# Kernel optimization log

Hardware: AMD Instinct MI355X
Metric: run time of the kernel (lower is better)

## Reference

```python
import jax, jax.numpy as jnp
import numpy as np


def _proj(x_flat, W, scale, bias):
    # x_flat: [B, C, N]; 1x1 conv == per-pixel channel matmul, then eval-mode BN (affine) + ReLU
    y = jnp.einsum('oc,bcn->bon', W, x_flat)
    return jax.nn.relu(y * scale[None, :, None] + bias[None, :, None])


def setup_inputs() -> dict:
    key = jax.random.key(0)
    ks = jax.random.split(key, 11)
    B, C, H, W = 4, 256, 64, 64
    inp = {
        'query_feats': jax.random.normal(ks[0], (B, C, H, W), jnp.float32),
        'key_feats': jax.random.normal(ks[1], (B, C, H, W), jnp.float32),
        'Wq': jax.random.normal(ks[2], (C, C), jnp.float32) * (1.0 / np.sqrt(C)),
        'Wk': jax.random.normal(ks[3], (C, C), jnp.float32) * (1.0 / np.sqrt(C)),
        'Wv': jax.random.normal(ks[4], (C, C), jnp.float32) * (1.0 / np.sqrt(C)),
        'scale_q': jax.random.uniform(ks[5], (C,), jnp.float32, 0.5, 1.5),
        'bias_q': jax.random.normal(ks[6], (C,), jnp.float32) * 0.1,
        'scale_k': jax.random.uniform(ks[7], (C,), jnp.float32, 0.5, 1.5),
        'bias_k': jax.random.normal(ks[8], (C,), jnp.float32) * 0.1,
        'scale_v': jax.random.uniform(ks[9], (C,), jnp.float32, 0.5, 1.5),
        'bias_v': jax.random.normal(ks[10], (C,), jnp.float32) * 0.1,
    }
    return inp


def reference(query_feats, key_feats, Wq, Wk, Wv, scale_q, bias_q, scale_k, bias_k, scale_v, bias_v):
    B, C, H, W = query_feats.shape
    qf = query_feats.reshape(B, C, H * W)
    kf = key_feats.reshape(B, C, H * W)

    q = _proj(qf, Wq, scale_q, bias_q)           # [B, C, Nq]
    k = _proj(kf, Wk, scale_k, bias_k)           # [B, C, Nk]
    v = _proj(kf, Wv, scale_v, bias_v)           # [B, C, Nk]

    sim = jnp.einsum('bcq,bck->bqk', q, k) * (C ** -0.5)  # [B, Nq, Nk]
    attn = jax.nn.softmax(sim, axis=-1)
    ctx = jnp.einsum('bqk,bck->bcq', attn, v)              # [B, C, Nq]
    return ctx.reshape(B, C, H, W)
```

## Files before the change

### kernel.cpp

```cpp
#include <hip/hip_runtime.h>
#include <math.h>

#define CDIM 256
#define NPIX 4096
#define BATCH 4
#define QB 64
#define KB 32

typedef __attribute__((ext_vector_type(8))) short short8;
typedef __attribute__((ext_vector_type(4))) float f32x4;
#define MFMA(a, b, c) __builtin_amdgcn_mfma_f32_16x16x32_bf16((a), (b), (c), 0, 0, 0)

__device__ __forceinline__ unsigned short f2bf(float f) {
    union { float f; unsigned int u; } v; v.f = f;
    unsigned int u = v.u;
    return (unsigned short)((u + 0x7FFFu + ((u >> 16) & 1u)) >> 16);
}
__device__ __forceinline__ float bf2f(unsigned short h) {
    union { unsigned int u; float f; } v; v.u = ((unsigned int)h) << 16;
    return v.f;
}

__global__ __launch_bounds__(256) void proj_kernel(
    const float* __restrict__ qf, const float* __restrict__ kf,
    const float* __restrict__ Wq, const float* __restrict__ Wk, const float* __restrict__ Wv,
    const float* __restrict__ sq, const float* __restrict__ bq,
    const float* __restrict__ sk, const float* __restrict__ bk,
    const float* __restrict__ sv, const float* __restrict__ bv,
    unsigned short* __restrict__ Qth, unsigned short* __restrict__ Qtl,
    unsigned short* __restrict__ Kth, unsigned short* __restrict__ Ktl,
    unsigned short* __restrict__ Vh,  unsigned short* __restrict__ Vl)
{
    const int n0 = blockIdx.x * 64;
    const int o0 = blockIdx.y * 64;
    const int z  = blockIdx.z;
    const int which = z % 3;
    const int b     = z / 3;

    const float* W; const float* x; const float* sc; const float* bi;
    unsigned short* dh; unsigned short* dl;
    if (which == 0)      { W = Wq; x = qf; sc = sq; bi = bq; dh = Qth; dl = Qtl; }
    else if (which == 1) { W = Wk; x = kf; sc = sk; bi = bk; dh = Kth; dl = Ktl; }
    else                 { W = Wv; x = kf; sc = sv; bi = bv; dh = Vh;  dl = Vl;  }

    __shared__ float Wt[32][68];
    __shared__ float Xt[32][68];

    const int t  = threadIdx.x;
    const int to = t >> 4;
    const int tn = t & 15;

    const int w_oi  = t >> 2;
    const int w_cc0 = (t & 3) * 8;
    const int x_ci  = t >> 3;
    const int x_no  = (t & 7) * 8;

    float acc[4][4];
#pragma unroll
    for (int i = 0; i < 4; ++i)
#pragma unroll
        for (int j = 0; j < 4; ++j) acc[i][j] = 0.f;

    for (int c0 = 0; c0 < CDIM; c0 += 32) {
        float4 wv[2], xv[2];
#pragma unroll
        for (int v = 0; v < 2; ++v)
            wv[v] = *reinterpret_cast<const float4*>(
                &W[(size_t)(o0 + w_oi) * CDIM + c0 + w_cc0 + 4 * v]);
#pragma unroll
        for (int v = 0; v < 2; ++v)
            xv[v] = *reinterpret_cast<const float4*>(
                &x[((size_t)(b * CDIM + c0 + x_ci)) * NPIX + n0 + x_no + 4 * v]);
        __syncthreads();
#pragma unroll
        for (int v = 0; v < 2; ++v) {
            Wt[w_cc0 + 4 * v + 0][w_oi] = wv[v].x;
            Wt[w_cc0 + 4 * v + 1][w_oi] = wv[v].y;
            Wt[w_cc0 + 4 * v + 2][w_oi] = wv[v].z;
            Wt[w_cc0 + 4 * v + 3][w_oi] = wv[v].w;
            *reinterpret_cast<float4*>(&Xt[x_ci][x_no + 4 * v]) = xv[v];
        }
        __syncthreads();
#pragma unroll
        for (int cc = 0; cc < 32; ++cc) {
            float4 a = *reinterpret_cast<const float4*>(&Wt[cc][4 * to]);
            float4 c = *reinterpret_cast<const float4*>(&Xt[cc][4 * tn]);
            float wa[4] = {a.x, a.y, a.z, a.w};
            float xa[4] = {c.x, c.y, c.z, c.w};
#pragma unroll
            for (int i = 0; i < 4; ++i)
#pragma unroll
                for (int j = 0; j < 4; ++j)
                    acc[i][j] = fmaf(wa[i], xa[j], acc[i][j]);
        }
        __syncthreads();
    }

    unsigned short hi[4][4], lo[4][4];
#pragma unroll
    for (int i = 0; i < 4; ++i) {
        const int o = o0 + 4 * to + i;
        const float s = sc[o], bb = bi[o];
#pragma unroll
        for (int j = 0; j < 4; ++j) {
            float val = fmaxf(fmaf(acc[i][j], s, bb), 0.f);
            unsigned short h = f2bf(val);
            hi[i][j] = h;
            lo[i][j] = f2bf(val - bf2f(h));
        }
    }

    if (which < 2) {
#pragma unroll
        for (int j = 0; j < 4; ++j) {
            const size_t addr = ((size_t)b * NPIX + n0 + 4 * tn + j) * CDIM + o0 + 4 * to;
            ushort4 h4 = make_ushort4(hi[0][j], hi[1][j], hi[2][j], hi[3][j]);
            ushort4 l4 = make_ushort4(lo[0][j], lo[1][j], lo[2][j], lo[3][j]);
            *reinterpret_cast<ushort4*>(&dh[addr]) = h4;
            *reinterpret_cast<ushort4*>(&dl[addr]) = l4;
        }
    } else {
#pragma unroll
        for (int i = 0; i < 4; ++i) {
            const size_t addr = ((size_t)b * CDIM + o0 + 4 * to + i) * NPIX + n0 + 4 * tn;
            ushort4 h4 = make_ushort4(hi[i][0], hi[i][1], hi[i][2], hi[i][3]);
            ushort4 l4 = make_ushort4(lo[i][0], lo[i][1], lo[i][2], lo[i][3]);
            *reinterpret_cast<ushort4*>(&dh[addr]) = h4;
            *reinterpret_cast<ushort4*>(&dl[addr]) = l4;
        }
    }
}

__global__ __launch_bounds__(512, 2) void flash_kernel(
    const unsigned short* __restrict__ Qth, const unsigned short* __restrict__ Qtl,
    const unsigned short* __restrict__ Kth, const unsigned short* __restrict__ Ktl,
    const unsigned short* __restrict__ Vh,  const unsigned short* __restrict__ Vl,
    float* __restrict__ out)
{
    const int bid  = blockIdx.x;
    const int virt = ((bid & 7) << 5) | (bid >> 3);
    const int b    = virt >> 6;
    const int qb   = (virt & 63) * QB;

    __shared__ unsigned short Ksh[KB][264], Ksl[KB][264];
    __shared__ unsigned short Vsh[CDIM][40], Vsl[CDIM][40];
    __shared__ unsigned short Phs[QB][40],  Pls[QB][40];
    __shared__ float Msh[2][QB], Ssh2[2][QB], Rsh[QB], Linv[QB];

    const int t    = threadIdx.x;
    const int w    = t >> 6;
    const int lane = t & 63;
    const int g    = lane >> 4;
    const int li   = lane & 15;

    const int smq = w & 3, snk = w >> 2;
    const int pqf = w & 3, pch = w >> 2;

    const int krow = t >> 4, kcol = (t & 15) * 16;
    const int vrow = t >> 1, vcol = (t & 1) * 16;

    short8 qh[8], ql[8];
    {
        const size_t qbase = ((size_t)b * NPIX + qb + smq * 16 + li) * CDIM + g * 8;
#pragma unroll
        for (int cs = 0; cs < 8; ++cs) {
            qh[cs] = *reinterpret_cast<const short8*>(&Qth[qbase + cs * 32]);
            ql[cs] = *reinterpret_cast<const short8*>(&Qtl[qbase + cs * 32]);
        }
    }

    f32x4 O[8];
#pragma unroll
    for (int fi = 0; fi < 8; ++fi) O[fi] = (f32x4){0.f, 0.f, 0.f, 0.f};

    float m_run[4], l_run[4];
#pragma unroll
    for (int r = 0; r < 4; ++r) { m_run[r] = -INFINITY; l_run[r] = 0.f; }

    const float scl = 0.0625f;

    uint4 rKh0, rKh1, rKl0, rKl1, rVh0, rVh1, rVl0, rVl1;
    const size_t kgbase = ((size_t)b * NPIX + krow) * CDIM + kcol;
    const size_t vgbase = ((size_t)b * CDIM + vrow) * NPIX + vcol;

    {
        const size_t ka = kgbase;
        rKh0 = *reinterpret_cast<const uint4*>(&Kth[ka]);
        rKh1 = *reinterpret_cast<const uint4*>(&Kth[ka + 8]);
        rKl0 = *reinterpret_cast<const uint4*>(&Ktl[ka]);
        rKl1 = *reinterpret_cast<const uint4*>(&Ktl[ka + 8]);
        const size_t va = vgbase;
        rVh0 = *reinterpret_cast<const uint4*>(&Vh[va]);
        rVh1 = *reinterpret_cast<const uint4*>(&Vh[va + 8]);
        rVl0 = *reinterpret_cast<const uint4*>(&Vl[va]);
        rVl1 = *reinterpret_cast<const uint4*>(&Vl[va + 8]);
    }

    const int NT = NPIX / KB;
    for (int it = 0; it < NT; ++it) {
        *reinterpret_cast<uint4*>(&Ksh[krow][kcol])     = rKh0;
        *reinterpret_cast<uint4*>(&Ksh[krow][kcol + 8]) = rKh1;
        *reinterpret_cast<uint4*>(&Ksl[krow][kcol])     = rKl0;
        *reinterpret_cast<uint4*>(&Ksl[krow][kcol + 8]) = rKl1;
        *reinterpret_cast<uint4*>(&Vsh[vrow][vcol])     = rVh0;
        *reinterpret_cast<uint4*>(&Vsh[vrow][vcol + 8]) = rVh1;
        *reinterpret_cast<uint4*>(&Vsl[vrow][vcol])     = rVl0;
        *reinterpret_cast<uint4*>(&Vsl[vrow][vcol + 8]) = rVl1;
        __syncthreads();

        f32x4 sacc = (f32x4){0.f, 0.f, 0.f, 0.f};
#pragma unroll
        for (int cs = 0; cs < 8; ++cs) {
            short8 kbh = *reinterpret_cast<const short8*>(&Ksh[snk * 16 + li][cs * 32 + g * 8]);
            short8 kbl = *reinterpret_cast<const short8*>(&Ksl[snk * 16 + li][cs * 32 + g * 8]);
            sacc = MFMA(qh[cs], kbh, sacc);
            sacc = MFMA(ql[cs], kbh, sacc);
            sacc = MFMA(qh[cs], kbl, sacc);
        }

        {
            const int ktn = (it + 1 < NT) ? (it + 1) * KB : 0;
            const size_t ka = kgbase + (size_t)ktn * CDIM;
            rKh0 = *reinterpret_cast<const uint4*>(&Kth[ka]);
            rKh1 = *reinterpret_cast<const uint4*>(&Kth[ka + 8]);
            rKl0 = *reinterpret_cast<const uint4*>(&Ktl[ka]);
            rKl1 = *reinterpret_cast<const uint4*>(&Ktl[ka + 8]);
            const size_t va = vgbase + ktn;
            rVh0 = *reinterpret_cast<const uint4*>(&Vh[va]);
            rVh1 = *reinterpret_cast<const uint4*>(&Vh[va + 8]);
            rVl0 = *reinterpret_cast<const uint4*>(&Vl[va]);
            rVl1 = *reinterpret_cast<const uint4*>(&Vl[va + 8]);
        }

        float sv[4], mx[4];
#pragma unroll
        for (int r = 0; r < 4; ++r) { sv[r] = sacc[r] * scl; mx[r] = sv[r]; }
#pragma unroll
        for (int d = 1; d < 16; d <<= 1)
#pragma unroll
            for (int r = 0; r < 4; ++r) mx[r] = fmaxf(mx[r], __shfl_xor(mx[r], d, 64));

        if (li == 0) {
#pragma unroll
            for (int r = 0; r < 4; ++r) Msh[snk][smq * 16 + g * 4 + r] = mx[r];
        }
        __syncthreads();

        float p[4], resc[4], psum[4];
#pragma unroll
        for (int r = 0; r < 4; ++r) {
            const int q = smq * 16 + g * 4 + r;
            const float mt = fmaxf(Msh[0][q], Msh[1][q]);
            const float mn = fmaxf(m_run[r], mt);
            resc[r] = __expf(m_run[r] - mn);
            m_run[r] = mn;
            p[r] = __expf(sv[r] - mn);
            psum[r] = p[r];
        }
#pragma unroll
        for (int d = 1; d < 16; d <<= 1)
#pragma unroll
            for (int r = 0; r < 4; ++r) psum[r] += __shfl_xor(psum[r], d, 64);

#pragma unroll
        for (int r = 0; r < 4; ++r) {
            const int q = smq * 16 + g * 4 + r;
            unsigned short ph = f2bf(p[r]);
            Phs[q][snk * 16 + li] = ph;
            Pls[q][snk * 16 + li] = f2bf(p[r] - bf2f(ph));
        }
        if (li == 0) {
#pragma unroll
            for (int r = 0; r < 4; ++r) {
                const int q = smq * 16 + g * 4 + r;
                Ssh2[snk][q] = psum[r];
                if (snk == 0) Rsh[q] = resc[r];
            }
        }
        __syncthreads();

#pragma unroll
        for (int r = 0; r < 4; ++r) {
            const int q = smq * 16 + g * 4 + r;
            l_run[r] = l_run[r] * resc[r] + Ssh2[0][q] + Ssh2[1][q];
        }

        const float rf = Rsh[pqf * 16 + li];
        short8 pa = *reinterpret_cast<const short8*>(&Phs[pqf * 16 + li][g * 8]);
        short8 pb = *reinterpret_cast<const short8*>(&Pls[pqf * 16 + li][g * 8]);
#pragma unroll
        for (int fi = 0; fi < 8; ++fi) {
            O[fi] = O[fi] * rf;
            const int crow = (pch * 8 + fi) * 16 + li;
            short8 va = *reinterpret_cast<const short8*>(&Vsh[crow][g * 8]);
            short8 vb = *reinterpret_cast<const short8*>(&Vsl[crow][g * 8]);
            O[fi] = MFMA(va, pa, O[fi]);
            O[fi] = MFMA(vb, pa, O[fi]);
            O[fi] = MFMA(va, pb, O[fi]);
        }
        __syncthreads();
    }

    if (snk == 0 && li == 0) {
#pragma unroll
        for (int r = 0; r < 4; ++r)
            Linv[smq * 16 + g * 4 + r] = 1.0f / l_run[r];
    }
    __syncthreads();

    const float linv = Linv[pqf * 16 + li];
#pragma unroll
    for (int fi = 0; fi < 8; ++fi) {
#pragma unroll
        for (int r = 0; r < 4; ++r) {
            const int c = (pch * 8 + fi) * 16 + g * 4 + r;
            out[((size_t)(b * CDIM + c)) * NPIX + qb + pqf * 16 + li] = O[fi][r] * linv;
        }
    }
}

extern "C" void kernel_launch(void* const* d_in, const int* in_sizes, int n_in,
                              void* d_out, int out_size, void* d_ws, size_t ws_size,
                              hipStream_t stream)
{
    const float* qf = (const float*)d_in[0];
    const float* kf = (const float*)d_in[1];
    const float* Wq = (const float*)d_in[2];
    const float* Wk = (const float*)d_in[3];
    const float* Wv = (const float*)d_in[4];
    const float* sq = (const float*)d_in[5];
    const float* bq = (const float*)d_in[6];
    const float* sk = (const float*)d_in[7];
    const float* bk = (const float*)d_in[8];
    const float* sv = (const float*)d_in[9];
    const float* bv = (const float*)d_in[10];
    float* out = (float*)d_out;

    const size_t plane = (size_t)BATCH * CDIM * NPIX;
    unsigned short* ws = (unsigned short*)d_ws;
    unsigned short* Qth = ws;
    unsigned short* Qtl = ws + plane;
    unsigned short* Kth = ws + 2 * plane;
    unsigned short* Ktl = ws + 3 * plane;
    unsigned short* Vh  = ws + 4 * plane;
    unsigned short* Vl  = ws + 5 * plane;

    dim3 gp(NPIX / 64, CDIM / 64, 3 * BATCH);
    proj_kernel<<<gp, 256, 0, stream>>>(qf, kf, Wq, Wk, Wv, sq, bq, sk, bk, sv, bv,
                                        Qth, Qtl, Kth, Ktl, Vh, Vl);

    flash_kernel<<<dim3(256), 512, 0, stream>>>(Qth, Qtl, Kth, Ktl, Vh, Vl, out);
}
```

Before: 590.3 us.

## Split KV range across two blocks with merge kernel and swizzle V shared layout

Splits the key/value sequence into two halves so the flash kernel launches 512 blocks instead of 256, writing unnormalized partial outputs plus running max and sum to workspace. A separate merge kernel then combines the two partials with log-sum-exp rescaling. The launch bound is raised to 4 blocks per SM, and the V shared tile drops its padding in favour of an XOR swizzle to avoid bank conflicts. This fills more compute units on a 256-CU GPU, at the cost of extra global traffic for the partials and an additional kernel launch. It falls back to the old path if the workspace is too small.

```diff
diff --git a/kernel.cpp b/kernel.cpp
--- a/kernel.cpp
+++ b/kernel.cpp
@@ -6,6 +6,7 @@
 #define BATCH 4
 #define QB 64
 #define KB 32
+#define KVHALF 2048
 
 typedef __attribute__((ext_vector_type(8))) short short8;
 typedef __attribute__((ext_vector_type(4))) float f32x4;
@@ -131,19 +132,30 @@
     }
 }
 
-__global__ __launch_bounds__(512, 2) void flash_kernel(
+__global__ __launch_bounds__(512, 4) void flash_kernel(
     const unsigned short* __restrict__ Qth, const unsigned short* __restrict__ Qtl,
     const unsigned short* __restrict__ Kth, const unsigned short* __restrict__ Ktl,
     const unsigned short* __restrict__ Vh,  const unsigned short* __restrict__ Vl,
-    float* __restrict__ out)
+    float* __restrict__ Op, float* __restrict__ Mp, float* __restrict__ Lp,
+    float* __restrict__ out, int split)
 {
-    const int bid  = blockIdx.x;
-    const int virt = ((bid & 7) << 5) | (bid >> 3);
-    const int b    = virt >> 6;
-    const int qb   = (virt & 63) * QB;
+    const int bid = blockIdx.x;
+    int qt, b, kv, ntiles;
+    if (split) {
+        const int virt = ((bid & 7) << 6) | (bid >> 3);
+        qt = virt & 63;
+        const int bkv = virt >> 6;
+        b = bkv >> 1; kv = bkv & 1; ntiles = KVHALF / KB;
+    } else {
+        const int virt = ((bid & 7) << 5) | (bid >> 3);
+        qt = virt & 63; b = virt >> 6; kv = 0; ntiles = NPIX / KB;
+    }
+    const int qb = qt * QB;
+    const int k0 = kv * KVHALF;
+    const int pb = b * 64 + qt;
 
     __shared__ unsigned short Ksh[KB][264], Ksl[KB][264];
-    __shared__ unsigned short Vsh[CDIM][40], Vsl[CDIM][40];
+    __shared__ unsigned short Vsh[CDIM][32], Vsl[CDIM][32];
     __shared__ unsigned short Phs[QB][40],  Pls[QB][40];
     __shared__ float Msh[2][QB], Ssh2[2][QB], Rsh[QB], Linv[QB];
 
@@ -158,6 +170,10 @@
 
     const int krow = t >> 4, kcol = (t & 15) * 16;
     const int vrow = t >> 1, vcol = (t & 1) * 16;
+    const int vsw  = (vrow >> 2) & 3;
+    const int vp0  = ((2 * (t & 1) + 0) ^ vsw) * 8;
+    const int vp1  = ((2 * (t & 1) + 1) ^ vsw) * 8;
+    const int pg   = (g ^ ((li >> 2) & 3)) * 8;
 
     short8 qh[8], ql[8];
     {
@@ -180,32 +196,29 @@
     const float scl = 0.0625f;
 
     uint4 rKh0, rKh1, rKl0, rKl1, rVh0, rVh1, rVl0, rVl1;
-    const size_t kgbase = ((size_t)b * NPIX + krow) * CDIM + kcol;
-    const size_t vgbase = ((size_t)b * CDIM + vrow) * NPIX + vcol;
-
-    {
-        const size_t ka = kgbase;
-        rKh0 = *reinterpret_cast<const uint4*>(&Kth[ka]);
-        rKh1 = *reinterpret_cast<const uint4*>(&Kth[ka + 8]);
-        rKl0 = *reinterpret_cast<const uint4*>(&Ktl[ka]);
-        rKl1 = *reinterpret_cast<const uint4*>(&Ktl[ka + 8]);
-        const size_t va = vgbase;
-        rVh0 = *reinterpret_cast<const uint4*>(&Vh[va]);
-        rVh1 = *reinterpret_cast<const uint4*>(&Vh[va + 8]);
-        rVl0 = *reinterpret_cast<const uint4*>(&Vl[va]);
-        rVl1 = *reinterpret_cast<const uint4*>(&Vl[va + 8]);
-    }
-
-    const int NT = NPIX / KB;
-    for (int it = 0; it < NT; ++it) {
+    const size_t kgbase = ((size_t)b * NPIX + k0 + krow) * CDIM + kcol;
+    const size_t vgbase = ((size_t)(b * CDIM + vrow)) * NPIX + k0 + vcol;
+
+    {
+        rKh0 = *reinterpret_cast<const uint4*>(&Kth[kgbase]);
+        rKh1 = *reinterpret_cast<const uint4*>(&Kth[kgbase + 8]);
+        rKl0 = *reinterpret_cast<const uint4*>(&Ktl[kgbase]);
+        rKl1 = *reinterpret_cast<const uint4*>(&Ktl[kgbase + 8]);
+        rVh0 = *reinterpret_cast<const uint4*>(&Vh[vgbase]);
+        rVh1 = *reinterpret_cast<const uint4*>(&Vh[vgbase + 8]);
+        rVl0 = *reinterpret_cast<const uint4*>(&Vl[vgbase]);
+        rVl1 = *reinterpret_cast<const uint4*>(&Vl[vgbase + 8]);
+    }
+
+    for (int it = 0; it < ntiles; ++it) {
         *reinterpret_cast<uint4*>(&Ksh[krow][kcol])     = rKh0;
         *reinterpret_cast<uint4*>(&Ksh[krow][kcol + 8]) = rKh1;
         *reinterpret_cast<uint4*>(&Ksl[krow][kcol])     = rKl0;
         *reinterpret_cast<uint4*>(&Ksl[krow][kcol + 8]) = rKl1;
-        *reinterpret_cast<uint4*>(&Vsh[vrow][vcol])     = rVh0;
-        *reinterpret_cast<uint4*>(&Vsh[vrow][vcol + 8]) = rVh1;
-        *reinterpret_cast<uint4*>(&Vsl[vrow][vcol])     = rVl0;
-        *reinterpret_cast<uint4*>(&Vsl[vrow][vcol + 8]) = rVl1;
+        *reinterpret_cast<uint4*>(&Vsh[vrow][vp0])      = rVh0;
+        *reinterpret_cast<uint4*>(&Vsh[vrow][vp1])      = rVh1;
+        *reinterpret_cast<uint4*>(&Vsl[vrow][vp0])      = rVl0;
+        *reinterpret_cast<uint4*>(&Vsl[vrow][vp1])      = rVl1;
         __syncthreads();
 
         f32x4 sacc = (f32x4){0.f, 0.f, 0.f, 0.f};
@@ -219,7 +232,7 @@
         }
 
         {
-            const int ktn = (it + 1 < NT) ? (it + 1) * KB : 0;
+            const int ktn = (it + 1 < ntiles) ? (it + 1) * KB : 0;
             const size_t ka = kgbase + (size_t)ktn * CDIM;
             rKh0 = *reinterpret_cast<const uint4*>(&Kth[ka]);
             rKh1 = *reinterpret_cast<const uint4*>(&Kth[ka + 8]);
@@ -287,36 +300,100 @@
 
         const float rf = Rsh[pqf * 16 + li];
         short8 pa = *reinterpret_cast<const short8*>(&Phs[pqf * 16 + li][g * 8]);
-        short8 pb = *reinterpret_cast<const short8*>(&Pls[pqf * 16 + li][g * 8]);
+        short8 pb2 = *reinterpret_cast<const short8*>(&Pls[pqf * 16 + li][g * 8]);
 #pragma unroll
         for (int fi = 0; fi < 8; ++fi) {
             O[fi] = O[fi] * rf;
             const int crow = (pch * 8 + fi) * 16 + li;
-            short8 va = *reinterpret_cast<const short8*>(&Vsh[crow][g * 8]);
-            short8 vb = *reinterpret_cast<const short8*>(&Vsl[crow][g * 8]);
+            short8 va = *reinterpret_cast<const short8*>(&Vsh[crow][pg]);
+            short8 vb = *reinterpret_cast<const short8*>(&Vsl[crow][pg]);
             O[fi] = MFMA(va, pa, O[fi]);
             O[fi] = MFMA(vb, pa, O[fi]);
-            O[fi] = MFMA(va, pb, O[fi]);
-        }
-        __syncthreads();
-    }
-
-    if (snk == 0 && li == 0) {
-#pragma unroll
-        for (int r = 0; r < 4; ++r)
-            Linv[smq * 16 + g * 4 + r] = 1.0f / l_run[r];
-    }
-    __syncthreads();
-
-    const float linv = Linv[pqf * 16 + li];
-#pragma unroll
-    for (int fi = 0; fi < 8; ++fi) {
-#pragma unroll
-        for (int r = 0; r < 4; ++r) {
-            const int c = (pch * 8 + fi) * 16 + g * 4 + r;
-            out[((size_t)(b * CDIM + c)) * NPIX + qb + pqf * 16 + li] = O[fi][r] * linv;
-        }
-    }
+            O[fi] = MFMA(va, pb2, O[fi]);
+        }
+        __syncthreads();
+    }
+
+    if (split) {
+        const size_t obase = ((size_t)(kv * 256 + pb)) * 256;
+#pragma unroll
+        for (int fi = 0; fi < 8; ++fi) {
+#pragma unroll
+            for (int r = 0; r < 4; ++r) {
+                const int c = (pch * 8 + fi) * 16 + g * 4 + r;
+                Op[(obase + c) * 64 + pqf * 16 + li] = O[fi][r];
+            }
+        }
+        if (snk == 0 && li == 0) {
+            const size_t mlbase = ((size_t)(kv * 256 + pb)) * 64;
+#pragma unroll
+            for (int r = 0; r < 4; ++r) {
+                const int q = smq * 16 + g * 4 + r;
+                Mp[mlbase + q] = m_run[r];
+                Lp[mlbase + q] = l_run[r];
+            }
+        }
+    } else {
+        if (snk == 0 && li == 0) {
+#pragma unroll
+            for (int r = 0; r < 4; ++r)
+                Linv[smq * 16 + g * 4 + r] = 1.0f / l_run[r];
+        }
+        __syncthreads();
+        const float linv = Linv[pqf * 16 + li];
+#pragma unroll
+        for (int fi = 0; fi < 8; ++fi) {
+#pragma unroll
+            for (int r = 0; r < 4; ++r) {
+                const int c = (pch * 8 + fi) * 16 + g * 4 + r;
+                out[((size_t)(b * CDIM + c)) * NPIX + qb + pqf * 16 + li] = O[fi][r] * linv;
+            }
+        }
+    }
+}
+
+__global__ __launch_bounds__(256) void merge_kernel(
+    const float* __restrict__ Op, const float* __restrict__ Mp, const float* __restrict__ Lp,
+    float* __restrict__ out)
+{
+    const int idx = blockIdx.x * 256 + threadIdx.x;
+    const int qq4 = idx & 15;
+    const int c   = (idx >> 4) & 255;
+    const int pb  = idx >> 12;
+    const int b   = pb >> 6;
+    const int qt  = pb & 63;
+
+    const size_t o0 = (((size_t)pb) * 256 + c) * 64 + qq4 * 4;
+    const size_t o1 = (((size_t)(256 + pb)) * 256 + c) * 64 + qq4 * 4;
+    float4 v0 = *reinterpret_cast<const float4*>(&Op[o0]);
+    float4 v1 = *reinterpret_cast<const float4*>(&Op[o1]);
+
+    const size_t ml0 = ((size_t)pb) * 64 + qq4 * 4;
+    const size_t ml1 = ((size_t)(256 + pb)) * 64 + qq4 * 4;
+    float4 m0 = *reinterpret_cast<const float4*>(&Mp[ml0]);
+    float4 m1 = *reinterpret_cast<const float4*>(&Mp[ml1]);
+    float4 l0 = *reinterpret_cast<const float4*>(&Lp[ml0]);
+    float4 l1 = *reinterpret_cast<const float4*>(&Lp[ml1]);
+
+    float4 r;
+    {
+        float M = fmaxf(m0.x, m1.x), a0 = __expf(m0.x - M), a1 = __expf(m1.x - M);
+        r.x = (v0.x * a0 + v1.x * a1) / (l0.x * a0 + l1.x * a1);
+    }
+    {
+        float M = fmaxf(m0.y, m1.y), a0 = __expf(m0.y - M), a1 = __expf(m1.y - M);
+        r.y = (v0.y * a0 + v1.y * a1) / (l0.y * a0 + l1.y * a1);
+    }
+    {
+        float M = fmaxf(m0.z, m1.z), a0 = __expf(m0.z - M), a1 = __expf(m1.z - M);
+        r.z = (v0.z * a0 + v1.z * a1) / (l0.z * a0 + l1.z * a1);
+    }
+    {
+        float M = fmaxf(m0.w, m1.w), a0 = __expf(m0.w - M), a1 = __expf(m1.w - M);
+        r.w = (v0.w * a0 + v1.w * a1) / (l0.w * a0 + l1.w * a1);
+    }
+
+    *reinterpret_cast<float4*>(&out[((size_t)(b * CDIM + c)) * NPIX + qt * 64 + qq4 * 4]) = r;
 }
 
 extern "C" void kernel_launch(void* const* d_in, const int* in_sizes, int n_in,
@@ -344,10 +421,24 @@
     unsigned short* Ktl = ws + 3 * plane;
     unsigned short* Vh  = ws + 4 * plane;
     unsigned short* Vl  = ws + 5 * plane;
+    float* Op = (float*)(ws + 6 * plane);
+    float* Mp = Op + (size_t)512 * 256 * 64;
+    float* Lp = Mp + (size_t)512 * 64;
+
+    const size_t need = 6 * plane * sizeof(unsigned short)
+                      + ((size_t)512 * 256 * 64 + 2 * (size_t)512 * 64) * sizeof(float);
+    const int split = (ws_size >= need) ? 1 : 0;
 
     dim3 gp(NPIX / 64, CDIM / 64, 3 * BATCH);
     proj_kernel<<<gp, 256, 0, stream>>>(qf, kf, Wq, Wk, Wv, sq, bq, sk, bk, sv, bv,
                                         Qth, Qtl, Kth, Ktl, Vh, Vl);
 
-    flash_kernel<<<dim3(256), 512, 0, stream>>>(Qth, Qtl, Kth, Ktl, Vh, Vl, out);
-}
+    if (split) {
+        flash_kernel<<<dim3(512), 512, 0, stream>>>(Qth, Qtl, Kth, Ktl, Vh, Vl,
+                                                    Op, Mp, Lp, out, 1);
+        merge_kernel<<<dim3(4096), 256, 0, stream>>>(Op, Mp, Lp, out);
+    } else {
+        flash_kernel<<<dim3(256), 512, 0, stream>>>(Qth, Qtl, Kth, Ktl, Vh, Vl,
+                                                    Op, Mp, Lp, out, 0);
+    }
+}
```

After: 925.4 us. 56.8% more time.
